# Performance work log

Measured on AMD Instinct MI355X. Metric: run time of the kernel, lower is better.

Reference implementation:

```python
import jax, jax.numpy as jnp
import numpy as np

DIM, HEADS, HEAD_DIM = 1024, 16, 64
B, S = 2, 1024
LAMBDA = 4.0
EPS = 1e-6


def setup_inputs() -> dict:
    key = jax.random.key(0)
    ks = jax.random.split(key, 7)
    sc = 1.0 / np.sqrt(DIM)
    return {
        "x": jax.random.normal(ks[0], (B, S, DIM), jnp.float32),
        "qkv_w": jax.random.normal(ks[1], (3 * DIM, DIM), jnp.float32) * sc,
        "qkv_b": jax.random.normal(ks[2], (3 * DIM,), jnp.float32) * 0.01,
        "proj_w": jax.random.normal(ks[3], (DIM, DIM), jnp.float32) * sc,
        "proj_b": jax.random.normal(ks[4], (DIM,), jnp.float32) * 0.01,
        "dwc_w": jax.random.normal(ks[5], (DIM, 1, 3), jnp.float32) * 0.3,
        "dwc_b": jax.random.normal(ks[6], (DIM,), jnp.float32) * 0.01,
    }


def _l1_dist(q, k):
    # q,k: [B,H,S,Dh] -> pairwise L1 distance [B,H,S,S].
    # Accumulate over head_dim with a (rematerialized) scan so we never
    # materialize the [B,H,S,S,Dh] broadcast tensor.
    qT = jnp.moveaxis(q, -1, 0)  # [Dh,B,H,S]
    kT = jnp.moveaxis(k, -1, 0)

    def step(acc, qk):
        qd, kd = qk  # [B,H,S]
        return acc + jnp.abs(qd[..., :, None] - kd[..., None, :]), None

    init = jnp.zeros(q.shape[:-1] + (k.shape[-2],), q.dtype)
    dist, _ = jax.lax.scan(jax.checkpoint(step), init, (qT, kT))
    return dist


def reference(x, qkv_w, qkv_b, proj_w, proj_b, dwc_w, dwc_b):
    Bq, Sq, C = x.shape
    # qkv projection -> q,k,v each [B,H,S,Dh]
    qkv = (x @ qkv_w.T + qkv_b).reshape(Bq, Sq, 3, HEADS, HEAD_DIM)
    qkv = jnp.transpose(qkv, (2, 0, 3, 1, 4))
    q, k, v = qkv[0], qkv[1], qkv[2]

    # exact Laplacian (L1-distance) kernel attention, row-normalized
    dist = _l1_dist(q, k)                       # [B,H,S,S]
    kern = jnp.exp(-LAMBDA * dist / HEAD_DIM)   # mean-L1 scaling
    attn = kern / (jnp.sum(kern, axis=-1, keepdims=True) + EPS)
    global_attn = jnp.einsum("bhij,bhjd->bhid", attn, v)

    # depthwise conv1d local branch on v (channel order = head-major)
    v1d = jnp.transpose(v, (0, 1, 3, 2)).reshape(Bq, C, Sq)  # [B,C,S]
    local = jax.lax.conv_general_dilated(
        v1d, dwc_w, window_strides=(1,), padding=((1, 1),),
        feature_group_count=C, dimension_numbers=("NCH", "OIH", "NCH"))
    local = local + dwc_b[None, :, None]
    local = jnp.transpose(local.reshape(Bq, HEADS, HEAD_DIM, Sq), (0, 1, 3, 2))

    y = global_attn + local                      # [B,H,S,Dh]
    y = jnp.transpose(y, (0, 2, 1, 3)).reshape(Bq, Sq, C)
    return y @ proj_w.T + proj_b
```

## Files before the change

kernel.cpp:

```cpp
#include <hip/hip_runtime.h>

#define DIMC 1024
#define HEADS 16
#define HD 64
#define BATCH 2
#define SEQ 1024
#define NQKV 3072

typedef _Float16 f16;
typedef _Float16 half8 __attribute__((ext_vector_type(8)));
typedef _Float16 half4v __attribute__((ext_vector_type(4)));
typedef float floatx4 __attribute__((ext_vector_type(4)));

__device__ __forceinline__ void gld16(const void* g, void* l) {
  __builtin_amdgcn_global_load_lds((const __attribute__((address_space(1))) void*)g,
                                   (__attribute__((address_space(3))) void*)l, 16, 0, 0);
}

__device__ __forceinline__ unsigned sadU8(unsigned a, unsigned b, unsigned c) {
#if __has_builtin(__builtin_amdgcn_sad_u8)
  return __builtin_amdgcn_sad_u8(a, b, c);
#else
  unsigned d;
  asm("v_sad_u8 %0, %1, %2, %3" : "=v"(d) : "v"(a), "v"(b), "v"(c));
  return d;
#endif
}

__global__ __launch_bounds__(256) void cvt_kernel(
    const float* __restrict__ x, const float* __restrict__ wq, const float* __restrict__ wp,
    f16* __restrict__ x16, f16* __restrict__ wq16, f16* __restrict__ wp16)
{
  int bid = blockIdx.x;
  const float* src; f16* dst; int base;
  if (bid < 512)        { src = x;  dst = x16;  base = bid; }
  else if (bid < 1280)  { src = wq; dst = wq16; base = bid - 512; }
  else                  { src = wp; dst = wp16; base = bid - 1280; }
  long long i0 = (long long)base*1024 + threadIdx.x;
#pragma unroll
  for (int k2 = 0; k2 < 4; ++k2) {
    long long i = i0 + k2*256;
    float4 v = ((const float4*)src)[i];
    half4v h; h[0]=(f16)v.x; h[1]=(f16)v.y; h[2]=(f16)v.z; h[3]=(f16)v.w;
    *(half4v*)(dst + i*4) = h;
  }
}

template<int TM, int TN, int BK, int MW, int MODE>
__global__ __launch_bounds__(256, MW) void gemm_kernel(
    const f16* __restrict__ A, const f16* __restrict__ Bw, const float* __restrict__ bias,
    unsigned char* __restrict__ q8, unsigned char* __restrict__ k8, f16* __restrict__ vT,
    float* __restrict__ outp, int K)
{
  constexpr int MT = TM / 32;
  constexpr int NT = TN / 32;
  constexpr int G  = BK / 8;
  __shared__ f16 As[TM*BK];
  __shared__ f16 Bs[TN*BK];
  const int tid = threadIdx.x;
  const int wave = tid >> 6, lane = tid & 63;
  const int lq = lane >> 4, li = lane & 15;
  const int m0 = blockIdx.y * TM, n0 = blockIdx.x * TN;
  const int wm = (wave & 1) * (TM/2), wn = (wave >> 1) * (TN/2);
  floatx4 acc[MT][NT] = {};

  const int kIters = K / BK;
  for (int kt = 0; kt < kIters; ++kt) {
    __syncthreads();
#pragma unroll
    for (int r = 0; r < TM*BK/2048; ++r) {
      int slot = r*256 + tid;
      int row = slot / G, c = slot % G, g = c ^ (row & (G-1));
      gld16(A + (size_t)(m0+row)*K + kt*BK + g*8, As + slot*8);
    }
#pragma unroll
    for (int r = 0; r < TN*BK/2048; ++r) {
      int slot = r*256 + tid;
      int row = slot / G, c = slot % G, g = c ^ (row & (G-1));
      gld16(Bw + (size_t)(n0+row)*K + kt*BK + g*8, Bs + slot*8);
    }
    __syncthreads();
#pragma unroll
    for (int ks = 0; ks < BK/32; ++ks) {
      half8 af[MT], bf[NT];
      int kc = ks*4 + lq;
#pragma unroll
      for (int t = 0; t < MT; ++t) {
        int am = wm + t*16 + li;
        af[t] = *(const half8*)&As[am*BK + (kc ^ (am & (G-1)))*8];
      }
#pragma unroll
      for (int t = 0; t < NT; ++t) {
        int bn = wn + t*16 + li;
        bf[t] = *(const half8*)&Bs[bn*BK + (kc ^ (bn & (G-1)))*8];
      }
#pragma unroll
      for (int mt = 0; mt < MT; ++mt)
#pragma unroll
        for (int nt = 0; nt < NT; ++nt)
          acc[mt][nt] = __builtin_amdgcn_mfma_f32_16x16x32_f16(af[mt], bf[nt], acc[mt][nt], 0, 0, 0);
    }
  }

#pragma unroll
  for (int mt = 0; mt < MT; ++mt) {
#pragma unroll
    for (int nt = 0; nt < NT; ++nt) {
      int f = n0 + wn + nt*16 + li;
      float bb = bias[f];
      if (MODE == 0) {
        int which = f >> 10, cc = f & 1023, h = cc >> 6, d = cc & 63;
        int t0 = m0 + wm + mt*16 + lq*4;
        int b = t0 >> 10, s0 = t0 & 1023;
        if (which == 2) {
          half4v hv;
#pragma unroll
          for (int r = 0; r < 4; ++r) hv[r] = (f16)(acc[mt][nt][r] + bb);
          *(half4v*)&vT[((size_t)((b*HEADS + h)*HD + d))*SEQ + s0] = hv;
        } else {
          unsigned char* dst = (which == 0) ? q8 : k8;
#pragma unroll
          for (int r = 0; r < 4; ++r) {
            float v = acc[mt][nt][r] + bb;
            int u = (int)floorf(v * 16.0f + 128.5f);
            u = u < 0 ? 0 : (u > 255 ? 255 : u);
            dst[((size_t)((b*HEADS + h)*SEQ + s0 + r))*HD + d] = (unsigned char)u;
          }
        }
      } else {
#pragma unroll
        for (int r = 0; r < 4; ++r) {
          int t = m0 + wm + mt*16 + lq*4 + r;
          outp[(size_t)t*DIMC + f] = acc[mt][nt][r] + bb;
        }
      }
    }
  }
}

__global__ __launch_bounds__(256, 3) void attn_kernel(
    const unsigned char* __restrict__ q8g, const unsigned char* __restrict__ k8g,
    const f16* __restrict__ vTg, const float* __restrict__ dwcw, const float* __restrict__ dwcb,
    f16* __restrict__ y16)
{
  __shared__ unsigned char q8s[64*64];
  __shared__ unsigned char k8s[128*64];
  __shared__ f16 vTs[64*128];
  __shared__ f16 sfrag[16*64*8];
  __shared__ float rspart[64*16];
  __shared__ float rowsum[64];

  const int tid = threadIdx.x;
  const int lin = blockIdx.x + 16 * blockIdx.y;
  const int bh = (lin & 7) * 4 + ((lin >> 3) & 3);
  const int i0 = (lin >> 5) * 64;
  const int lane = tid & 63, wave = tid >> 6;
  const int lq = lane >> 4, li = lane & 15;
  const int iL = tid & 15, jt = tid >> 4;
  const int ksj = jt >> 2, qj = jt & 3;

  {
    gld16(q8g + ((size_t)(bh*SEQ) + i0)*HD + tid*16, q8s + tid*16);
  }
  __syncthreads();

  unsigned qr[4][16];
#pragma unroll
  for (int n = 0; n < 4; ++n)
#pragma unroll
    for (int c4 = 0; c4 < 4; ++c4) {
      uint4 t = *(const uint4*)&q8s[(iL + n*16)*64 + c4*16];
      qr[n][c4*4+0] = t.x; qr[n][c4*4+1] = t.y; qr[n][c4*4+2] = t.z; qr[n][c4*4+3] = t.w;
    }

  float rs[4] = {0.f, 0.f, 0.f, 0.f};
  floatx4 pacc[2][2] = {};
  const int mtb = (wave & 1) * 2, ntb = (wave >> 1) * 2;

  for (int jb = 0; jb < 8; ++jb) {
    const int j0 = jb * 128;
    __syncthreads();
#pragma unroll
    for (int r = 0; r < 2; ++r) {
      int slot = r*256 + tid;
      gld16(k8g + ((size_t)(bh*SEQ) + j0)*HD + slot*16, k8s + slot*16);
    }
#pragma unroll
    for (int r = 0; r < 4; ++r) {
      int slot = r*256 + tid;
      int d = slot >> 4, c = slot & 15, sc = c ^ (d & 7);
      gld16(vTg + ((size_t)(bh*HD) + d)*SEQ + j0 + sc*8, vTs + slot*8);
    }
    __syncthreads();

    unsigned sacc[4][8] = {};
#pragma unroll
    for (int c4 = 0; c4 < 4; ++c4) {
      uint4 kk[8];
#pragma unroll
      for (int jj = 0; jj < 8; ++jj)
        kk[jj] = *(const uint4*)&k8s[(jt*8 + jj)*64 + c4*16];
#pragma unroll
      for (int n = 0; n < 4; ++n)
#pragma unroll
        for (int jj = 0; jj < 8; ++jj) {
          sacc[n][jj] = sadU8(qr[n][c4*4+0], kk[jj].x, sacc[n][jj]);
          sacc[n][jj] = sadU8(qr[n][c4*4+1], kk[jj].y, sacc[n][jj]);
          sacc[n][jj] = sadU8(qr[n][c4*4+2], kk[jj].z, sacc[n][jj]);
          sacc[n][jj] = sadU8(qr[n][c4*4+3], kk[jj].w, sacc[n][jj]);
        }
    }
#pragma unroll
    for (int n = 0; n < 4; ++n) {
      half8 sv;
#pragma unroll
      for (int jj = 0; jj < 8; ++jj) {
        float sf = exp2f(-0.0056355275f * (float)sacc[n][jj]);
        rs[n] += sf;
        sv[jj] = (f16)sf;
      }
      *(half8*)&sfrag[((n*4 + ksj)*64 + qj*16 + iL)*8] = sv;
    }
    __syncthreads();

#pragma unroll
    for (int ks = 0; ks < 4; ++ks) {
      half8 a0 = *(const half8*)&sfrag[(((mtb+0)*4 + ks)*64 + lane)*8];
      half8 a1 = *(const half8*)&sfrag[(((mtb+1)*4 + ks)*64 + lane)*8];
#pragma unroll
      for (int nt = 0; nt < 2; ++nt) {
        int d = (ntb + nt)*16 + li;
        int kc = ks*4 + lq;
        half8 bfr = *(const half8*)&vTs[d*128 + (kc ^ (d & 7))*8];
        pacc[0][nt] = __builtin_amdgcn_mfma_f32_16x16x32_f16(a0, bfr, pacc[0][nt], 0, 0, 0);
        pacc[1][nt] = __builtin_amdgcn_mfma_f32_16x16x32_f16(a1, bfr, pacc[1][nt], 0, 0, 0);
      }
    }
  }

#pragma unroll
  for (int n = 0; n < 4; ++n) rspart[(iL + n*16)*16 + jt] = rs[n];
  __syncthreads();
  if (tid < 64) {
    float s = 0.f;
#pragma unroll
    for (int t = 0; t < 16; ++t) s += rspart[tid*16 + t];
    rowsum[tid] = s + 1e-6f;
  }
  __syncthreads();

  const int b = bh >> 4, h = bh & 15;
#pragma unroll
  for (int nt = 0; nt < 2; ++nt) {
    int d = (ntb + nt)*16 + li;
    int c = h*64 + d;
    float w0 = dwcw[c*3+0], w1 = dwcw[c*3+1], w2 = dwcw[c*3+2], cb = dwcb[c];
    const f16* vrow = vTg + ((size_t)(bh*HD) + d)*SEQ;
#pragma unroll
    for (int mt = 0; mt < 2; ++mt) {
      int s0 = i0 + (mtb + mt)*16 + lq*4;
      float vv[6];
#pragma unroll
      for (int e = 0; e < 6; ++e) {
        int s = s0 - 1 + e;
        vv[e] = (s >= 0 && s < SEQ) ? (float)vrow[s] : 0.f;
      }
#pragma unroll
      for (int r = 0; r < 4; ++r) {
        int ii = (mtb + mt)*16 + lq*4 + r;
        float val = pacc[mt][nt][r] / rowsum[ii];
        val += w0*vv[r] + w1*vv[r+1] + w2*vv[r+2] + cb;
        int s = i0 + ii;
        y16[((size_t)(b*SEQ + s))*DIMC + c] = (f16)val;
      }
    }
  }
}

extern "C" void kernel_launch(void* const* d_in, const int* in_sizes, int n_in,
                              void* d_out, int out_size, void* d_ws, size_t ws_size,
                              hipStream_t stream) {
  const float* x      = (const float*)d_in[0];
  const float* qkv_w  = (const float*)d_in[1];
  const float* qkv_b  = (const float*)d_in[2];
  const float* proj_w = (const float*)d_in[3];
  const float* proj_b = (const float*)d_in[4];
  const float* dwc_w  = (const float*)d_in[5];
  const float* dwc_b  = (const float*)d_in[6];
  float* out = (float*)d_out;

  char* ws = (char*)d_ws;
  f16* x16  = (f16*)(ws);
  f16* wq16 = (f16*)(ws + (4ll<<20));
  f16* wp16 = (f16*)(ws + (10ll<<20));
  unsigned char* q8 = (unsigned char*)(ws + (12ll<<20));
  unsigned char* k8 = (unsigned char*)(ws + (14ll<<20));
  f16* vT   = (f16*)(ws + (16ll<<20));
  f16* y16  = (f16*)(ws + (20ll<<20));

  cvt_kernel<<<1536, 256, 0, stream>>>(x, qkv_w, proj_w, x16, wq16, wp16);
  gemm_kernel<128,128,64,3,0><<<dim3(24, 16), 256, 0, stream>>>(x16, wq16, qkv_b, q8, k8, vT, nullptr, DIMC);
  attn_kernel<<<dim3(16, 32), 256, 0, stream>>>(q8, k8, vT, dwc_w, dwc_b, y16);
  gemm_kernel<64,64,128,4,1><<<dim3(16, 32), 256, 0, stream>>>(y16, wp16, proj_b, nullptr, nullptr, nullptr, out, DIMC);
}
```

Baseline: 153.8 us.

## Halve attention query tile to 32 rows and retune QKV GEMM tiling

The attention kernel now handles 32 query rows per block instead of 64. The grid doubles to 1024 blocks, each wave owns one 16-wide slice of head_dim, and launch bounds rise to 4 blocks per CU for more occupancy and more even load across CUs. In exchange, every K/V tile is loaded from global memory twice as often per query row, so the SAD work per K load is halved. The QKV GEMM template also changes its K-tile and stage parameters (64,3 to 128,2).

```diff
diff --git a/kernel.cpp b/kernel.cpp
--- a/kernel.cpp
+++ b/kernel.cpp
@@ -138,44 +138,44 @@
   }
 }
 
-__global__ __launch_bounds__(256, 3) void attn_kernel(
+__global__ __launch_bounds__(256, 4) void attn_kernel(
     const unsigned char* __restrict__ q8g, const unsigned char* __restrict__ k8g,
     const f16* __restrict__ vTg, const float* __restrict__ dwcw, const float* __restrict__ dwcb,
     f16* __restrict__ y16)
 {
-  __shared__ unsigned char q8s[64*64];
+  __shared__ unsigned char q8s[32*64];
   __shared__ unsigned char k8s[128*64];
   __shared__ f16 vTs[64*128];
-  __shared__ f16 sfrag[16*64*8];
-  __shared__ float rspart[64*16];
-  __shared__ float rowsum[64];
+  __shared__ f16 sfrag[8*64*8];
+  __shared__ float rspart[32*16];
+  __shared__ float rowsum[32];
 
   const int tid = threadIdx.x;
   const int lin = blockIdx.x + 16 * blockIdx.y;
   const int bh = (lin & 7) * 4 + ((lin >> 3) & 3);
-  const int i0 = (lin >> 5) * 64;
+  const int i0 = (lin >> 5) * 32;
   const int lane = tid & 63, wave = tid >> 6;
   const int lq = lane >> 4, li = lane & 15;
   const int iL = tid & 15, jt = tid >> 4;
   const int ksj = jt >> 2, qj = jt & 3;
 
   {
-    gld16(q8g + ((size_t)(bh*SEQ) + i0)*HD + tid*16, q8s + tid*16);
+    if (tid < 128)
+      gld16(q8g + ((size_t)(bh*SEQ) + i0)*HD + tid*16, q8s + tid*16);
   }
   __syncthreads();
 
-  unsigned qr[4][16];
-#pragma unroll
-  for (int n = 0; n < 4; ++n)
+  unsigned qr[2][16];
+#pragma unroll
+  for (int n = 0; n < 2; ++n)
 #pragma unroll
     for (int c4 = 0; c4 < 4; ++c4) {
       uint4 t = *(const uint4*)&q8s[(iL + n*16)*64 + c4*16];
       qr[n][c4*4+0] = t.x; qr[n][c4*4+1] = t.y; qr[n][c4*4+2] = t.z; qr[n][c4*4+3] = t.w;
     }
 
-  float rs[4] = {0.f, 0.f, 0.f, 0.f};
-  floatx4 pacc[2][2] = {};
-  const int mtb = (wave & 1) * 2, ntb = (wave >> 1) * 2;
+  float rs[2] = {0.f, 0.f};
+  floatx4 pacc[2] = {};
 
   for (int jb = 0; jb < 8; ++jb) {
     const int j0 = jb * 128;
@@ -193,7 +193,7 @@
     }
     __syncthreads();
 
-    unsigned sacc[4][8] = {};
+    unsigned sacc[2][8] = {};
 #pragma unroll
     for (int c4 = 0; c4 < 4; ++c4) {
       uint4 kk[8];
@@ -201,7 +201,7 @@
       for (int jj = 0; jj < 8; ++jj)
         kk[jj] = *(const uint4*)&k8s[(jt*8 + jj)*64 + c4*16];
 #pragma unroll
-      for (int n = 0; n < 4; ++n)
+      for (int n = 0; n < 2; ++n)
 #pragma unroll
         for (int jj = 0; jj < 8; ++jj) {
           sacc[n][jj] = sadU8(qr[n][c4*4+0], kk[jj].x, sacc[n][jj]);
@@ -211,7 +211,7 @@
         }
     }
 #pragma unroll
-    for (int n = 0; n < 4; ++n) {
+    for (int n = 0; n < 2; ++n) {
       half8 sv;
 #pragma unroll
       for (int jj = 0; jj < 8; ++jj) {
@@ -225,23 +225,20 @@
 
 #pragma unroll
     for (int ks = 0; ks < 4; ++ks) {
-      half8 a0 = *(const half8*)&sfrag[(((mtb+0)*4 + ks)*64 + lane)*8];
-      half8 a1 = *(const half8*)&sfrag[(((mtb+1)*4 + ks)*64 + lane)*8];
-#pragma unroll
-      for (int nt = 0; nt < 2; ++nt) {
-        int d = (ntb + nt)*16 + li;
-        int kc = ks*4 + lq;
-        half8 bfr = *(const half8*)&vTs[d*128 + (kc ^ (d & 7))*8];
-        pacc[0][nt] = __builtin_amdgcn_mfma_f32_16x16x32_f16(a0, bfr, pacc[0][nt], 0, 0, 0);
-        pacc[1][nt] = __builtin_amdgcn_mfma_f32_16x16x32_f16(a1, bfr, pacc[1][nt], 0, 0, 0);
-      }
-    }
-  }
-
-#pragma unroll
-  for (int n = 0; n < 4; ++n) rspart[(iL + n*16)*16 + jt] = rs[n];
+      half8 a0 = *(const half8*)&sfrag[((0*4 + ks)*64 + lane)*8];
+      half8 a1 = *(const half8*)&sfrag[((1*4 + ks)*64 + lane)*8];
+      int d = wave*16 + li;
+      int kc = ks*4 + lq;
+      half8 bfr = *(const half8*)&vTs[d*128 + (kc ^ (d & 7))*8];
+      pacc[0] = __builtin_amdgcn_mfma_f32_16x16x32_f16(a0, bfr, pacc[0], 0, 0, 0);
+      pacc[1] = __builtin_amdgcn_mfma_f32_16x16x32_f16(a1, bfr, pacc[1], 0, 0, 0);
+    }
+  }
+
+#pragma unroll
+  for (int n = 0; n < 2; ++n) rspart[(iL + n*16)*16 + jt] = rs[n];
   __syncthreads();
-  if (tid < 64) {
+  if (tid < 32) {
     float s = 0.f;
 #pragma unroll
     for (int t = 0; t < 16; ++t) s += rspart[tid*16 + t];
@@ -250,15 +247,14 @@
   __syncthreads();
 
   const int b = bh >> 4, h = bh & 15;
-#pragma unroll
-  for (int nt = 0; nt < 2; ++nt) {
-    int d = (ntb + nt)*16 + li;
+  {
+    int d = wave*16 + li;
     int c = h*64 + d;
     float w0 = dwcw[c*3+0], w1 = dwcw[c*3+1], w2 = dwcw[c*3+2], cb = dwcb[c];
     const f16* vrow = vTg + ((size_t)(bh*HD) + d)*SEQ;
 #pragma unroll
     for (int mt = 0; mt < 2; ++mt) {
-      int s0 = i0 + (mtb + mt)*16 + lq*4;
+      int s0 = i0 + mt*16 + lq*4;
       float vv[6];
 #pragma unroll
       for (int e = 0; e < 6; ++e) {
@@ -267,8 +263,8 @@
       }
 #pragma unroll
       for (int r = 0; r < 4; ++r) {
-        int ii = (mtb + mt)*16 + lq*4 + r;
-        float val = pacc[mt][nt][r] / rowsum[ii];
+        int ii = mt*16 + lq*4 + r;
+        float val = pacc[mt][r] / rowsum[ii];
         val += w0*vv[r] + w1*vv[r+1] + w2*vv[r+2] + cb;
         int s = i0 + ii;
         y16[((size_t)(b*SEQ + s))*DIMC + c] = (f16)val;
@@ -299,7 +295,7 @@
   f16* y16  = (f16*)(ws + (20ll<<20));
 
   cvt_kernel<<<1536, 256, 0, stream>>>(x, qkv_w, proj_w, x16, wq16, wp16);
-  gemm_kernel<128,128,64,3,0><<<dim3(24, 16), 256, 0, stream>>>(x16, wq16, qkv_b, q8, k8, vT, nullptr, DIMC);
-  attn_kernel<<<dim3(16, 32), 256, 0, stream>>>(q8, k8, vT, dwc_w, dwc_b, y16);
+  gemm_kernel<128,128,128,2,0><<<dim3(24, 16), 256, 0, stream>>>(x16, wq16, qkv_b, q8, k8, vT, nullptr, DIMC);
+  attn_kernel<<<dim3(16, 64), 256, 0, stream>>>(q8, k8, vT, dwc_w, dwc_b, y16);
   gemm_kernel<64,64,128,4,1><<<dim3(16, 32), 256, 0, stream>>>(y16, wp16, proj_b, nullptr, nullptr, nullptr, out, DIMC);
 }
```

Measured after the change: 150.1 us. 2.4% less time.
